# Kernel tuning notes

Measured on AMD Instinct MI355X. Metric: run time of the kernel, lower is better.

Reference implementation:

```python
import jax, jax.numpy as jnp
import numpy as np

B, S, H = 2, 2048, 1024
NH = 16
HD = H // NH
MLP = 32


def setup_inputs() -> dict:
    key = jax.random.key(0)
    ks = jax.random.split(key, 24)
    def lin(k, fan_in, shape):
        bound = 1.0 / np.sqrt(fan_in)
        return jax.random.uniform(k, shape, jnp.float32, -bound, bound)
    return {
        "hidden_states": jax.random.normal(ks[0], (B, S, H), jnp.float32),
        "importance_scores": jax.random.uniform(ks[1], (B, S), jnp.float32),
        "wq": lin(ks[2], H, (H, H)), "bq": lin(ks[3], H, (H,)),
        "wk": lin(ks[4], H, (H, H)), "bk": lin(ks[5], H, (H,)),
        "wv": lin(ks[6], H, (H, H)), "bv": lin(ks[7], H, (H,)),
        "wo": lin(ks[8], H, (H, H)), "bo": lin(ks[9], H, (H,)),
        "rw1": lin(ks[10], 1, (1, MLP)), "rb1": lin(ks[11], 1, (MLP,)),
        "rw2": lin(ks[12], MLP, (MLP, NH)), "rb2": lin(ks[13], MLP, (NH,)),
        "aw1": lin(ks[14], 1, (1, MLP)), "ab1": lin(ks[15], 1, (MLP,)),
        "aw2": lin(ks[16], MLP, (MLP, NH)), "ab2": lin(ks[17], MLP, (NH,)),
        "log_temperature": jnp.zeros((NH,), jnp.float32),
        "ln_g": jnp.ones((H,), jnp.float32),
        "ln_b": jnp.zeros((H,), jnp.float32),
    }


def _forward(hidden_states, importance_scores, wq, bq, wk, bk, wv, bv, wo, bo,
             rw1, rb1, rw2, rb2, aw1, ab1, aw2, ab2, log_temperature, ln_g, ln_b):
    Bs, Ss, Hs = hidden_states.shape
    # Q, K, V: (B, NH, S, HD)
    def proj(w, b):
        return (hidden_states @ w + b).reshape(Bs, Ss, NH, HD).transpose(0, 2, 1, 3)
    Q, K, V = proj(wq, bq), proj(wk, bk), proj(wv, bv)
    scale = jnp.sqrt(jnp.float32(HD))
    attn_logits = jnp.einsum('bhqd,bhkd->bhqk', Q, K) / scale

    imp = importance_scores[..., None]  # (B, S, 1)
    def mlp(w1, b1, w2, b2):
        h = jax.nn.gelu(imp @ w1 + b1, approximate=False)
        return h @ w2 + b2  # (B, S, NH)
    reach = mlp(rw1, rb1, rw2, rb2).transpose(0, 2, 1)[..., None]      # (B,NH,S,1)
    attract = mlp(aw1, ab1, aw2, ab2).transpose(0, 2, 1)[..., None, :]  # (B,NH,1,S)

    pos = jnp.arange(Ss, dtype=jnp.float32)
    dist = jnp.abs(pos[None, :] - pos[:, None])  # (S, S); matches |i-j| (symmetric)
    temperature = jnp.exp(log_temperature).reshape(1, NH, 1, 1) + 1.0
    normalized_dist = dist[None, None] / Ss
    mask_logits = reach + attract - normalized_dist / temperature
    mask_bias = jnp.log(jax.nn.sigmoid(mask_logits) + 1e-8)

    attn_weights = jax.nn.softmax(attn_logits + mask_bias, axis=-1)
    attn_out = jnp.einsum('bhqk,bhkd->bhqd', attn_weights, V)
    attn_out = attn_out.transpose(0, 2, 1, 3).reshape(Bs, Ss, Hs)
    out = attn_out @ wo + bo

    x = hidden_states + out
    mu = jnp.mean(x, axis=-1, keepdims=True)
    var = jnp.mean(jnp.square(x - mu), axis=-1, keepdims=True)
    return (x - mu) / jnp.sqrt(var + 1e-5) * ln_g + ln_b


def reference(hidden_states, importance_scores, wq, bq, wk, bk, wv, bv, wo, bo,
              rw1, rb1, rw2, rb2, aw1, ab1, aw2, ab2, log_temperature, ln_g, ln_b):
    return _forward(hidden_states, importance_scores, wq, bq, wk, bk, wv, bv, wo, bo,
                    rw1, rb1, rw2, rb2, aw1, ab1, aw2, ab2, log_temperature, ln_g, ln_b)
```

## Files before the change

### kernel.cpp

```cpp
#include <hip/hip_runtime.h>
#include <math.h>

#define NB 2
#define NS 2048
#define NHID 1024
#define NHEAD 16
#define DHEAD 64

typedef _Float16 half_t;
typedef _Float16 hx4 __attribute__((ext_vector_type(4)));
typedef _Float16 hx8 __attribute__((ext_vector_type(8)));
typedef float fx4 __attribute__((ext_vector_type(4)));

#define RLN2 1.4426950408889634f
#define SCALE_Q 0.18033688011112042f

typedef const __attribute__((address_space(1))) void* gvp;
typedef __attribute__((address_space(3))) void* svp;

static __device__ __forceinline__ void gload16(const void* g, void* s) {
  __builtin_amdgcn_global_load_lds((gvp)g, (svp)s, 16, 0, 0);
}

static __device__ __forceinline__ float gelu_exact(float x) {
  return 0.5f * x * (1.0f + erff(x * 0.70710678118654752f));
}

__launch_bounds__(256)
__global__ void prep(const float* __restrict__ x, half_t* __restrict__ xb,
                     const float* __restrict__ w0, const float* __restrict__ w1,
                     const float* __restrict__ w2, const float* __restrict__ w3,
                     half_t* __restrict__ o0, half_t* __restrict__ o1,
                     half_t* __restrict__ o2, half_t* __restrict__ o3) {
  __shared__ float tile[32][33];
  const int t = threadIdx.x;
  if (blockIdx.x < 4096) {
    const int i = blockIdx.x * 256 + t;
    const fx4 v = ((const fx4*)x)[i];
    hx4 o;
#pragma unroll
    for (int j = 0; j < 4; ++j) o[j] = (half_t)v[j];
    ((hx4*)xb)[i] = o;
    return;
  }
  const int bid = blockIdx.x - 4096;
  const int z = bid >> 10;
  const float* w = (z == 0) ? w0 : (z == 1) ? w1 : (z == 2) ? w2 : w3;
  half_t* o = (z == 0) ? o0 : (z == 1) ? o1 : (z == 2) ? o2 : o3;
  const int n0 = (bid & 31) * 32, k0 = ((bid >> 5) & 31) * 32;
  const int tx = t & 31, ty = t >> 5;
#pragma unroll
  for (int i = 0; i < 4; ++i)
    tile[ty + i * 8][tx] = w[(size_t)(k0 + ty + i * 8) * NHID + n0 + tx];
  __syncthreads();
#pragma unroll
  for (int i = 0; i < 4; ++i)
    o[(size_t)(n0 + ty + i * 8) * NHID + k0 + tx] = (half_t)tile[tx][ty + i * 8];
}

__launch_bounds__(256)
__global__ void mlp16(const float* __restrict__ imp,
                      const float* __restrict__ rw1, const float* __restrict__ rb1,
                      const float* __restrict__ rw2, const float* __restrict__ rb2,
                      const float* __restrict__ aw1, const float* __restrict__ ab1,
                      const float* __restrict__ aw2, const float* __restrict__ ab2,
                      const float* __restrict__ ltemp,
                      float* __restrict__ u1G, float* __restrict__ u2G,
                      float* __restrict__ eapG, float* __restrict__ eamG) {
  const int i = blockIdx.x * 256 + threadIdx.x;
  const float v = imp[i];
  const int b = i >> 11, s = i & (NS - 1);
  float ra[16] = {}, aa[16] = {};
  for (int m = 0; m < 32; ++m) {
    const float hr = gelu_exact(v * rw1[m] + rb1[m]);
    const float ha = gelu_exact(v * aw1[m] + ab1[m]);
#pragma unroll
    for (int h = 0; h < 16; ++h) {
      ra[h] += hr * rw2[m * 16 + h];
      aa[h] += ha * aw2[m * 16 + h];
    }
  }
  const float sf = (float)s;
#pragma unroll
  for (int h = 0; h < 16; ++h) {
    const float ndc2 = RLN2 / ((__expf(ltemp[h]) + 1.0f) * (float)NS);
    const float r = (ra[h] + rb2[h]) * RLN2;
    const float a = (aa[h] + ab2[h]) * RLN2;
    const size_t idx = (size_t)(b * NHEAD + h) * NS + s;
    u1G[idx]  = __builtin_amdgcn_exp2f(sf * ndc2 - r);
    u2G[idx]  = __builtin_amdgcn_exp2f(-sf * ndc2 - r);
    eapG[idx] = __builtin_amdgcn_exp2f(-a - sf * ndc2);
    eamG[idx] = __builtin_amdgcn_exp2f(-a + sf * ndc2);
  }
}

__launch_bounds__(256, 3)
__global__ void gemm_qkv(const half_t* __restrict__ A,
                         const half_t* __restrict__ Wq, const half_t* __restrict__ Wk,
                         const half_t* __restrict__ Wv,
                         const float* __restrict__ bq, const float* __restrict__ bk,
                         const float* __restrict__ bv,
                         half_t* __restrict__ Qo, half_t* __restrict__ Ko,
                         half_t* __restrict__ Vo) {
  __shared__ __align__(16) half_t As[128 * 32];
  __shared__ __align__(16) half_t Bs[128 * 32];
  const int z = blockIdx.z;
  const half_t* Bt = (z == 0) ? Wq : (z == 1) ? Wk : Wv;
  const float* bias = (z == 0) ? bq : (z == 1) ? bk : bv;
  half_t* Co = (z == 0) ? Qo : (z == 1) ? Ko : Vo;
  const float oscale = (z == 0) ? SCALE_Q : 1.0f;

  const int t = threadIdx.x;
  const int l = t & 63, w = t >> 6;
  const int lo = l & 15, g = l >> 4;
  const int m0 = blockIdx.x * 128, n0 = blockIdx.y * 128;
  const int wm = (w >> 1) * 64, wn = (w & 1) * 64;
  fx4 acc[4][4] = {};

  for (int k0 = 0; k0 < NHID; k0 += 32) {
#pragma unroll
    for (int i = 0; i < 2; ++i) {
      const int c = i * 256 + t;
      const int row = c >> 2, kc = (c & 3) * 8;
      gload16(A + (size_t)(m0 + row) * NHID + k0 + kc, As + c * 8);
      gload16(Bt + (size_t)(n0 + row) * NHID + k0 + kc, Bs + c * 8);
    }
    __syncthreads();
    hx8 af[4], bfv[4];
#pragma unroll
    for (int i = 0; i < 4; ++i) {
      af[i] = *(const hx8*)(As + (wm + i * 16 + lo) * 32 + g * 8);
      bfv[i] = *(const hx8*)(Bs + (wn + i * 16 + lo) * 32 + g * 8);
    }
#pragma unroll
    for (int mi = 0; mi < 4; ++mi)
#pragma unroll
      for (int ni = 0; ni < 4; ++ni)
        acc[mi][ni] = __builtin_amdgcn_mfma_f32_16x16x32_f16(af[mi], bfv[ni], acc[mi][ni], 0, 0, 0);
    __syncthreads();
  }

#pragma unroll
  for (int mi = 0; mi < 4; ++mi) {
    const int r0 = m0 + wm + mi * 16 + g * 4;
#pragma unroll
    for (int ni = 0; ni < 4; ++ni) {
      const int col = n0 + wn + ni * 16 + lo;
      const float bs = bias[col];
#pragma unroll
      for (int j = 0; j < 4; ++j)
        Co[(size_t)(r0 + j) * NHID + col] = (half_t)((acc[mi][ni][j] + bs) * oscale);
    }
  }
}

__launch_bounds__(256)
__global__ void vtrans(const half_t* __restrict__ in, half_t* __restrict__ out) {
  __shared__ half_t tile[64][72];
  const int b = blockIdx.z, s0 = blockIdx.x * 64, n0 = blockIdx.y * 64;
  const int t = threadIdx.x;
  const int r = t >> 3, c = (t & 7) * 8;
  const half_t* ip = in + ((size_t)(b * NS) + s0) * NHID + n0;
#pragma unroll
  for (int i = 0; i < 2; ++i)
    *(hx8*)&tile[r + i * 32][c] = *(const hx8*)(ip + (size_t)(r + i * 32) * NHID + c);
  __syncthreads();
  half_t* op = out + ((size_t)(b * NHID) + n0) * NS + s0;
#pragma unroll
  for (int i = 0; i < 2; ++i) {
    hx8 v;
#pragma unroll
    for (int j = 0; j < 8; ++j) v[j] = tile[c + j][r + i * 32];
    *(hx8*)(op + (size_t)(r + i * 32) * NS + c) = v;
  }
}

__launch_bounds__(256, 3)
__global__ void gemm_o(const half_t* __restrict__ A, const half_t* __restrict__ Bt,
                       const float* __restrict__ bias, const half_t* __restrict__ resid,
                       half_t* __restrict__ Yh) {
  __shared__ __align__(16) half_t As[128 * 32];
  __shared__ __align__(16) half_t Bs[128 * 32];
  const int t = threadIdx.x;
  const int l = t & 63, w = t >> 6;
  const int lo = l & 15, g = l >> 4;
  const int m0 = blockIdx.x * 128, n0 = blockIdx.y * 128;
  const int wm = (w >> 1) * 64, wn = (w & 1) * 64;
  fx4 acc[4][4] = {};

  for (int k0 = 0; k0 < NHID; k0 += 32) {
#pragma unroll
    for (int i = 0; i < 2; ++i) {
      const int c = i * 256 + t;
      const int row = c >> 2, kc = (c & 3) * 8;
      gload16(A + (size_t)(m0 + row) * NHID + k0 + kc, As + c * 8);
      gload16(Bt + (size_t)(n0 + row) * NHID + k0 + kc, Bs + c * 8);
    }
    __syncthreads();
    hx8 af[4], bfv[4];
#pragma unroll
    for (int i = 0; i < 4; ++i) {
      af[i] = *(const hx8*)(As + (wm + i * 16 + lo) * 32 + g * 8);
      bfv[i] = *(const hx8*)(Bs + (wn + i * 16 + lo) * 32 + g * 8);
    }
#pragma unroll
    for (int mi = 0; mi < 4; ++mi)
#pragma unroll
      for (int ni = 0; ni < 4; ++ni)
        acc[mi][ni] = __builtin_amdgcn_mfma_f32_16x16x32_f16(af[mi], bfv[ni], acc[mi][ni], 0, 0, 0);
    __syncthreads();
  }

#pragma unroll
  for (int mi = 0; mi < 4; ++mi) {
    const int r0 = m0 + wm + mi * 16 + g * 4;
#pragma unroll
    for (int ni = 0; ni < 4; ++ni) {
      const int col = n0 + wn + ni * 16 + lo;
      const float bs = bias[col];
#pragma unroll
      for (int j = 0; j < 4; ++j) {
        const size_t idx = (size_t)(r0 + j) * NHID + col;
        Yh[idx] = (half_t)(acc[mi][ni][j] + bs + (float)resid[idx]);
      }
    }
  }
}

__launch_bounds__(256, 4)
__global__ void attn64(const half_t* __restrict__ Qb, const half_t* __restrict__ Kb,
                       const half_t* __restrict__ Vtb,
                       const float* __restrict__ u1G, const float* __restrict__ u2G,
                       const float* __restrict__ eapG, const float* __restrict__ eamG,
                       half_t* __restrict__ O) {
  __shared__ __align__(16) half_t Ks[2][64 * 64];
  __shared__ __align__(16) half_t Vs[2][64 * 64];
  __shared__ float eapS[2][64], eamS[2][64];

  const int t = threadIdx.x;
  const int l = t & 63, w = t >> 6;
  const int lo = l & 15, g = l >> 4;
  const int id = blockIdx.x;
  const int swz = (id & 7) * 128 + (id >> 3);
  const int q0 = (swz & 31) * 64;
  const int bh = swz >> 5;
  const int b = bh >> 4;
  const int q = q0 + w * 16 + lo;

  const float u1 = u1G[(size_t)bh * NS + q];
  const float u2 = u2G[(size_t)bh * NS + q];

  hx8 qf[2];
  {
    const half_t* qp = Qb + (size_t)(b * NS + q) * NHID + (bh & 15) * DHEAD + g * 8;
    qf[0] = *(const hx8*)(qp);
    qf[1] = *(const hx8*)(qp + 32);
  }

  fx4 o[4] = {};
  float s_run = 0.0f;
  const auto one2 = __builtin_amdgcn_cvt_pkrtz(1.0f, 1.0f);

  const half_t* Kbase = Kb + (size_t)b * (NS * NHID) + (bh & 15) * DHEAD;
  const half_t* Vbase = Vtb + (size_t)bh * (DHEAD * NS);
  const float* eapb = eapG + (size_t)bh * NS;
  const float* eamb = eamG + (size_t)bh * NS;

#pragma unroll
  for (int i = 0; i < 2; ++i) {
    const int c = i * 256 + t;
    const int row = c >> 3;
    const int ca = (c & 7) ^ (row & 7);
    gload16(Kbase + (size_t)row * NHID + ca * 8, &Ks[0][c * 8]);
    gload16(Vbase + (size_t)row * NS + ca * 8, &Vs[0][c * 8]);
  }
  if (t < 64) eapS[0][t] = eapb[t];
  else if (t < 128) eamS[0][t - 64] = eamb[t - 64];
  __syncthreads();

  int buf = 0;
  for (int kv0 = 0; kv0 < NS; kv0 += 64, buf ^= 1) {
    if (kv0 + 64 < NS) {
      const int nb = buf ^ 1;
      const int kvn = kv0 + 64;
#pragma unroll
      for (int i = 0; i < 2; ++i) {
        const int c = i * 256 + t;
        const int row = c >> 3;
        const int ca = (c & 7) ^ (row & 7);
        gload16(Kbase + (size_t)(kvn + row) * NHID + ca * 8, &Ks[nb][c * 8]);
        gload16(Vbase + (size_t)row * NS + kvn + ca * 8, &Vs[nb][c * 8]);
      }
      if (t < 64) eapS[nb][t] = eapb[kvn + t];
      else if (t < 128) eamS[nb][t - 64] = eamb[kvn + t - 64];
    }

    fx4 sa[4] = {};
#pragma unroll
    for (int mf = 0; mf < 4; ++mf) {
      const int row = mf * 16 + lo;
      const half_t* kr = &Ks[buf][row * 64];
      const int rx = row & 7;
#pragma unroll
      for (int ks = 0; ks < 2; ++ks) {
        const hx8 kf = *(const hx8*)(kr + (((ks * 4 + g) ^ rx) * 8));
        sa[mf] = __builtin_amdgcn_mfma_f32_16x16x32_f16(kf, qf[ks], sa[mf], 0, 0, 0);
      }
    }

    float psum = s_run;
    hx4 pb[4];
#pragma unroll
    for (int mf = 0; mf < 4; ++mf) {
      const fx4 ea = *(const fx4*)&eapS[buf][mf * 16 + g * 4];
      const fx4 em = *(const fx4*)&eamS[buf][mf * 16 + g * 4];
      float pe[4];
#pragma unroll
      for (int j = 0; j < 4; ++j) {
        const float u = fmaxf(u1 * ea[j], u2 * em[j]);
        const float e = __builtin_amdgcn_exp2f(sa[mf][j]);
        pe[j] = e * __builtin_amdgcn_rcpf(1.0f + u);
      }
      const auto c0 = __builtin_amdgcn_cvt_pkrtz(pe[0], pe[1]);
      const auto c1 = __builtin_amdgcn_cvt_pkrtz(pe[2], pe[3]);
      psum = __builtin_amdgcn_fdot2(c0, one2, psum, false);
      psum = __builtin_amdgcn_fdot2(c1, one2, psum, false);
      pb[mf][0] = (half_t)c0[0]; pb[mf][1] = (half_t)c0[1];
      pb[mf][2] = (half_t)c1[0]; pb[mf][3] = (half_t)c1[1];
    }
    s_run = psum;

#pragma unroll
    for (int df = 0; df < 4; ++df) {
      const int r = df * 16 + lo;
      const half_t* vr = &Vs[buf][r * 64 + (g & 1) * 4];
      const int rx = r & 7;
#pragma unroll
      for (int mf = 0; mf < 4; ++mf) {
        const hx4 vf = *(const hx4*)(vr + (((2 * mf + (g >> 1)) ^ rx) * 8));
        o[df] = __builtin_amdgcn_mfma_f32_16x16x16f16(vf, pb[mf], o[df], 0, 0, 0);
      }
    }
    __syncthreads();
  }

  s_run += __shfl_xor(s_run, 16);
  s_run += __shfl_xor(s_run, 32);
  const float inv = 1.0f / s_run;
  half_t* ob = O + (size_t)(b * NS + q) * NHID + (bh & 15) * DHEAD + g * 4;
#pragma unroll
  for (int df = 0; df < 4; ++df) {
    hx4 v;
#pragma unroll
    for (int j = 0; j < 4; ++j) v[j] = (half_t)(o[df][j] * inv);
    *(hx4*)(ob + df * 16) = v;
  }
}

__launch_bounds__(256)
__global__ void lnorm(const half_t* __restrict__ y, const float* __restrict__ g,
                      const float* __restrict__ bta, float* __restrict__ out) {
  const int row = blockIdx.x;
  const int t = threadIdx.x;
  const hx4 vh = ((const hx4*)(y + (size_t)row * NHID))[t];
  fx4 v;
#pragma unroll
  for (int j = 0; j < 4; ++j) v[j] = (float)vh[j];
  float s = v[0] + v[1] + v[2] + v[3];
  float sq = v[0] * v[0] + v[1] * v[1] + v[2] * v[2] + v[3] * v[3];
#pragma unroll
  for (int off = 1; off < 64; off <<= 1) {
    s += __shfl_xor(s, off);
    sq += __shfl_xor(sq, off);
  }
  __shared__ float rs[4], rsq[4];
  const int w = t >> 6;
  if ((t & 63) == 0) { rs[w] = s; rsq[w] = sq; }
  __syncthreads();
  s = rs[0] + rs[1] + rs[2] + rs[3];
  sq = rsq[0] + rsq[1] + rsq[2] + rsq[3];
  const float mu = s * (1.0f / NHID);
  const float var = sq * (1.0f / NHID) - mu * mu;
  const float rstd = rsqrtf(fmaxf(var, 0.0f) + 1e-5f);
  const fx4 gg = ((const fx4*)g)[t];
  const fx4 bb = ((const fx4*)bta)[t];
  fx4 o;
#pragma unroll
  for (int j = 0; j < 4; ++j) o[j] = (v[j] - mu) * rstd * gg[j] + bb[j];
  ((fx4*)(out + (size_t)row * NHID))[t] = o;
}

extern "C" void kernel_launch(void* const* d_in, const int* in_sizes, int n_in,
                              void* d_out, int out_size, void* d_ws, size_t ws_size,
                              hipStream_t stream) {
  const float* hidden = (const float*)d_in[0];
  const float* imp = (const float*)d_in[1];
  const float* wq = (const float*)d_in[2];  const float* bq = (const float*)d_in[3];
  const float* wk = (const float*)d_in[4];  const float* bk = (const float*)d_in[5];
  const float* wv = (const float*)d_in[6];  const float* bv = (const float*)d_in[7];
  const float* wo = (const float*)d_in[8];  const float* bo = (const float*)d_in[9];
  const float* rw1 = (const float*)d_in[10]; const float* rb1 = (const float*)d_in[11];
  const float* rw2 = (const float*)d_in[12]; const float* rb2 = (const float*)d_in[13];
  const float* aw1 = (const float*)d_in[14]; const float* ab1 = (const float*)d_in[15];
  const float* aw2 = (const float*)d_in[16]; const float* ab2 = (const float*)d_in[17];
  const float* ltemp = (const float*)d_in[18];
  const float* lng = (const float*)d_in[19]; const float* lnb = (const float*)d_in[20];

  char* ws = (char*)d_ws;
  half_t* Xb  = (half_t*)(ws);
  half_t* Wqt = (half_t*)(ws + (size_t)(8u << 20));
  half_t* Wkt = (half_t*)(ws + (size_t)(10u << 20));
  half_t* Wvt = (half_t*)(ws + (size_t)(12u << 20));
  half_t* Wot = (half_t*)(ws + (size_t)(14u << 20));
  half_t* Qb  = (half_t*)(ws + (size_t)(16u << 20));
  half_t* Kb  = (half_t*)(ws + (size_t)(24u << 20));
  half_t* Vtb = (half_t*)(ws + (size_t)(32u << 20));
  half_t* Vb  = (half_t*)(ws + (size_t)(40u << 20));
  half_t* AO  = (half_t*)(ws + (size_t)(40u << 20));
  float*  u1G  = (float*)(ws + (size_t)(48u << 20));
  float*  u2G  = (float*)(ws + (size_t)(48u << 20) + 524288);
  float*  eapG = (float*)(ws + (size_t)(48u << 20) + 1048576);
  float*  eamG = (float*)(ws + (size_t)(48u << 20) + 1572864);
  half_t* Y = (half_t*)(ws + (size_t)(16u << 20));

  prep<<<dim3(8192), dim3(256), 0, stream>>>(hidden, Xb, wq, wk, wv, wo,
                                             Wqt, Wkt, Wvt, Wot);
  mlp16<<<dim3(16), dim3(256), 0, stream>>>(imp, rw1, rb1, rw2, rb2, aw1, ab1, aw2, ab2,
                                            ltemp, u1G, u2G, eapG, eamG);
  gemm_qkv<<<dim3(32, 8, 3), dim3(256), 0, stream>>>(Xb, Wqt, Wkt, Wvt, bq, bk, bv,
                                                     Qb, Kb, Vb);
  vtrans<<<dim3(32, 16, 2), dim3(256), 0, stream>>>(Vb, Vtb);
  attn64<<<dim3(1024), dim3(256), 0, stream>>>(Qb, Kb, Vtb, u1G, u2G, eapG, eamG, AO);
  gemm_o<<<dim3(32, 8), dim3(256), 0, stream>>>(AO, Wot, bo, Xb, Y);
  lnorm<<<dim3(4096), dim3(256), 0, stream>>>(Y, lng, lnb, (float*)d_out);
}
```

Before: 273.3 us.

## Single-buffer attention tiles for higher occupancy; fold MLP kernel into prep

The attention kernel drops its K/V/mask double buffering and keeps one LDS buffer. The next tile is loaded after compute, behind a barrier, and launch bounds are raised from 4 to 8 blocks per CU so other blocks can hide load latency instead. The small mlp16 kernel is merged into the prep launch as 16 extra blocks, removing one kernel launch. The cost is that load/compute overlap inside each block is lost, and register pressure under the tighter bound may cause spills.

Result: slower. 315.5 us (+15.4%).

```diff
diff --git a/kernel.cpp b/kernel.cpp
--- a/kernel.cpp
+++ b/kernel.cpp
@@ -31,7 +31,15 @@
                      const float* __restrict__ w0, const float* __restrict__ w1,
                      const float* __restrict__ w2, const float* __restrict__ w3,
                      half_t* __restrict__ o0, half_t* __restrict__ o1,
-                     half_t* __restrict__ o2, half_t* __restrict__ o3) {
+                     half_t* __restrict__ o2, half_t* __restrict__ o3,
+                     const float* __restrict__ imp,
+                     const float* __restrict__ rw1, const float* __restrict__ rb1,
+                     const float* __restrict__ rw2, const float* __restrict__ rb2,
+                     const float* __restrict__ aw1, const float* __restrict__ ab1,
+                     const float* __restrict__ aw2, const float* __restrict__ ab2,
+                     const float* __restrict__ ltemp,
+                     float* __restrict__ u1G, float* __restrict__ u2G,
+                     float* __restrict__ eapG, float* __restrict__ eamG) {
   __shared__ float tile[32][33];
   const int t = threadIdx.x;
   if (blockIdx.x < 4096) {
@@ -41,6 +49,34 @@
 #pragma unroll
     for (int j = 0; j < 4; ++j) o[j] = (half_t)v[j];
     ((hx4*)xb)[i] = o;
+    return;
+  }
+  if (blockIdx.x >= 8192) {
+    const int i = (blockIdx.x - 8192) * 256 + t;
+    const float v = imp[i];
+    const int b = i >> 11, s = i & (NS - 1);
+    float ra[16] = {}, aa[16] = {};
+    for (int m = 0; m < 32; ++m) {
+      const float hr = gelu_exact(v * rw1[m] + rb1[m]);
+      const float ha = gelu_exact(v * aw1[m] + ab1[m]);
+#pragma unroll
+      for (int h = 0; h < 16; ++h) {
+        ra[h] += hr * rw2[m * 16 + h];
+        aa[h] += ha * aw2[m * 16 + h];
+      }
+    }
+    const float sf = (float)s;
+#pragma unroll
+    for (int h = 0; h < 16; ++h) {
+      const float ndc2 = RLN2 / ((__expf(ltemp[h]) + 1.0f) * (float)NS);
+      const float r = (ra[h] + rb2[h]) * RLN2;
+      const float a = (aa[h] + ab2[h]) * RLN2;
+      const size_t idx = (size_t)(b * NHEAD + h) * NS + s;
+      u1G[idx]  = __builtin_amdgcn_exp2f(sf * ndc2 - r);
+      u2G[idx]  = __builtin_amdgcn_exp2f(-sf * ndc2 - r);
+      eapG[idx] = __builtin_amdgcn_exp2f(-a - sf * ndc2);
+      eamG[idx] = __builtin_amdgcn_exp2f(-a + sf * ndc2);
+    }
     return;
   }
   const int bid = blockIdx.x - 4096;
@@ -56,42 +92,6 @@
 #pragma unroll
   for (int i = 0; i < 4; ++i)
     o[(size_t)(n0 + ty + i * 8) * NHID + k0 + tx] = (half_t)tile[tx][ty + i * 8];
-}
-
-__launch_bounds__(256)
-__global__ void mlp16(const float* __restrict__ imp,
-                      const float* __restrict__ rw1, const float* __restrict__ rb1,
-                      const float* __restrict__ rw2, const float* __restrict__ rb2,
-                      const float* __restrict__ aw1, const float* __restrict__ ab1,
-                      const float* __restrict__ aw2, const float* __restrict__ ab2,
-                      const float* __restrict__ ltemp,
-                      float* __restrict__ u1G, float* __restrict__ u2G,
-                      float* __restrict__ eapG, float* __restrict__ eamG) {
-  const int i = blockIdx.x * 256 + threadIdx.x;
-  const float v = imp[i];
-  const int b = i >> 11, s = i & (NS - 1);
-  float ra[16] = {}, aa[16] = {};
-  for (int m = 0; m < 32; ++m) {
-    const float hr = gelu_exact(v * rw1[m] + rb1[m]);
-    const float ha = gelu_exact(v * aw1[m] + ab1[m]);
-#pragma unroll
-    for (int h = 0; h < 16; ++h) {
-      ra[h] += hr * rw2[m * 16 + h];
-      aa[h] += ha * aw2[m * 16 + h];
-    }
-  }
-  const float sf = (float)s;
-#pragma unroll
-  for (int h = 0; h < 16; ++h) {
-    const float ndc2 = RLN2 / ((__expf(ltemp[h]) + 1.0f) * (float)NS);
-    const float r = (ra[h] + rb2[h]) * RLN2;
-    const float a = (aa[h] + ab2[h]) * RLN2;
-    const size_t idx = (size_t)(b * NHEAD + h) * NS + s;
-    u1G[idx]  = __builtin_amdgcn_exp2f(sf * ndc2 - r);
-    u2G[idx]  = __builtin_amdgcn_exp2f(-sf * ndc2 - r);
-    eapG[idx] = __builtin_amdgcn_exp2f(-a - sf * ndc2);
-    eamG[idx] = __builtin_amdgcn_exp2f(-a + sf * ndc2);
-  }
 }
 
 __launch_bounds__(256, 3)
@@ -227,15 +227,15 @@
   }
 }
 
-__launch_bounds__(256, 4)
+__launch_bounds__(256, 8)
 __global__ void attn64(const half_t* __restrict__ Qb, const half_t* __restrict__ Kb,
                        const half_t* __restrict__ Vtb,
                        const float* __restrict__ u1G, const float* __restrict__ u2G,
                        const float* __restrict__ eapG, const float* __restrict__ eamG,
                        half_t* __restrict__ O) {
-  __shared__ __align__(16) half_t Ks[2][64 * 64];
-  __shared__ __align__(16) half_t Vs[2][64 * 64];
-  __shared__ float eapS[2][64], eamS[2][64];
+  __shared__ __align__(16) half_t Ks[64 * 64];
+  __shared__ __align__(16) half_t Vs[64 * 64];
+  __shared__ float eapS[64], eamS[64];
 
   const int t = threadIdx.x;
   const int l = t & 63, w = t >> 6;
@@ -271,35 +271,20 @@
     const int c = i * 256 + t;
     const int row = c >> 3;
     const int ca = (c & 7) ^ (row & 7);
-    gload16(Kbase + (size_t)row * NHID + ca * 8, &Ks[0][c * 8]);
-    gload16(Vbase + (size_t)row * NS + ca * 8, &Vs[0][c * 8]);
-  }
-  if (t < 64) eapS[0][t] = eapb[t];
-  else if (t < 128) eamS[0][t - 64] = eamb[t - 64];
-  __syncthreads();
-
-  int buf = 0;
-  for (int kv0 = 0; kv0 < NS; kv0 += 64, buf ^= 1) {
-    if (kv0 + 64 < NS) {
-      const int nb = buf ^ 1;
-      const int kvn = kv0 + 64;
-#pragma unroll
-      for (int i = 0; i < 2; ++i) {
-        const int c = i * 256 + t;
-        const int row = c >> 3;
-        const int ca = (c & 7) ^ (row & 7);
-        gload16(Kbase + (size_t)(kvn + row) * NHID + ca * 8, &Ks[nb][c * 8]);
-        gload16(Vbase + (size_t)row * NS + kvn + ca * 8, &Vs[nb][c * 8]);
-      }
-      if (t < 64) eapS[nb][t] = eapb[kvn + t];
-      else if (t < 128) eamS[nb][t - 64] = eamb[kvn + t - 64];
-    }
+    gload16(Kbase + (size_t)row * NHID + ca * 8, &Ks[c * 8]);
+    gload16(Vbase + (size_t)row * NS + ca * 8, &Vs[c * 8]);
+  }
+  if (t < 64) eapS[t] = eapb[t];
+  else if (t < 128) eamS[t - 64] = eamb[t - 64];
+
+  for (int kv0 = 0; kv0 < NS; kv0 += 64) {
+    __syncthreads();
 
     fx4 sa[4] = {};
 #pragma unroll
     for (int mf = 0; mf < 4; ++mf) {
       const int row = mf * 16 + lo;
-      const half_t* kr = &Ks[buf][row * 64];
+      const half_t* kr = &Ks[row * 64];
       const int rx = row & 7;
 #pragma unroll
       for (int ks = 0; ks < 2; ++ks) {
@@ -312,8 +297,8 @@
     hx4 pb[4];
 #pragma unroll
     for (int mf = 0; mf < 4; ++mf) {
-      const fx4 ea = *(const fx4*)&eapS[buf][mf * 16 + g * 4];
-      const fx4 em = *(const fx4*)&eamS[buf][mf * 16 + g * 4];
+      const fx4 ea = *(const fx4*)&eapS[mf * 16 + g * 4];
+      const fx4 em = *(const fx4*)&eamS[mf * 16 + g * 4];
       float pe[4];
 #pragma unroll
       for (int j = 0; j < 4; ++j) {
@@ -333,7 +318,7 @@
 #pragma unroll
     for (int df = 0; df < 4; ++df) {
       const int r = df * 16 + lo;
-      const half_t* vr = &Vs[buf][r * 64 + (g & 1) * 4];
+      const half_t* vr = &Vs[r * 64 + (g & 1) * 4];
       const int rx = r & 7;
 #pragma unroll
       for (int mf = 0; mf < 4; ++mf) {
@@ -342,6 +327,20 @@
       }
     }
     __syncthreads();
+
+    if (kv0 + 64 < NS) {
+      const int kvn = kv0 + 64;
+#pragma unroll
+      for (int i = 0; i < 2; ++i) {
+        const int c = i * 256 + t;
+        const int row = c >> 3;
+        const int ca = (c & 7) ^ (row & 7);
+        gload16(Kbase + (size_t)(kvn + row) * NHID + ca * 8, &Ks[c * 8]);
+        gload16(Vbase + (size_t)row * NS + kvn + ca * 8, &Vs[c * 8]);
+      }
+      if (t < 64) eapS[t] = eapb[kvn + t];
+      else if (t < 128) eamS[t - 64] = eamb[kvn + t - 64];
+    }
   }
 
   s_run += __shfl_xor(s_run, 16);
@@ -423,10 +422,11 @@
   float*  eamG = (float*)(ws + (size_t)(48u << 20) + 1572864);
   half_t* Y = (half_t*)(ws + (size_t)(16u << 20));
 
-  prep<<<dim3(8192), dim3(256), 0, stream>>>(hidden, Xb, wq, wk, wv, wo,
-                                             Wqt, Wkt, Wvt, Wot);
-  mlp16<<<dim3(16), dim3(256), 0, stream>>>(imp, rw1, rb1, rw2, rb2, aw1, ab1, aw2, ab2,
-                                            ltemp, u1G, u2G, eapG, eamG);
+  prep<<<dim3(8208), dim3(256), 0, stream>>>(hidden, Xb, wq, wk, wv, wo,
+                                             Wqt, Wkt, Wvt, Wot,
+                                             imp, rw1, rb1, rw2, rb2,
+                                             aw1, ab1, aw2, ab2, ltemp,
+                                             u1G, u2G, eapG, eamG);
   gemm_qkv<<<dim3(32, 8, 3), dim3(256), 0, stream>>>(Xb, Wqt, Wkt, Wvt, bq, bk, bv,
                                                      Qb, Kb, Vb);
   vtrans<<<dim3(32, 16, 2), dim3(256), 0, stream>>>(Vb, Vtb);
```
